# Optimization experiments

Measured on AMD Instinct MI355X. Metric: run time of the kernel, lower is better.

Reference implementation:

```python
import jax, jax.numpy as jnp
import numpy as np

EMBED_DIM = 768
NUM_HEADS = 12
HEAD_DIM = EMBED_DIM // NUM_HEADS
B, N = 4, 2048


def setup_inputs() -> dict:
    key = jax.random.key(0)
    k_x, k_wqkv, k_bqkv, k_wo, k_bo = jax.random.split(key, 5)
    s = 1.0 / np.sqrt(EMBED_DIM)
    return {
        "x": jax.random.normal(k_x, (B, N, EMBED_DIM), dtype=jnp.float32),
        # torch nn.Linear weight layout: [out_features, in_features]
        "w_qkv": jax.random.uniform(k_wqkv, (3 * EMBED_DIM, EMBED_DIM), minval=-s, maxval=s, dtype=jnp.float32),
        "b_qkv": jax.random.uniform(k_bqkv, (3 * EMBED_DIM,), minval=-s, maxval=s, dtype=jnp.float32),
        "w_out": jax.random.uniform(k_wo, (EMBED_DIM, EMBED_DIM), minval=-s, maxval=s, dtype=jnp.float32),
        "b_out": jax.random.uniform(k_bo, (EMBED_DIM,), minval=-s, maxval=s, dtype=jnp.float32),
    }


def reference(x, w_qkv, b_qkv, w_out, b_out):
    Bsz, Nlen, C = x.shape
    # fused QKV projection: [B, N, 3C]
    qkv = jnp.einsum("bnc,oc->bno", x, w_qkv) + b_qkv
    qkv = qkv.reshape(Bsz, Nlen, 3, NUM_HEADS, HEAD_DIM)
    q = qkv[:, :, 0].transpose(0, 2, 1, 3)  # [B, H, N, D]
    k = qkv[:, :, 1].transpose(0, 2, 1, 3)
    v = qkv[:, :, 2].transpose(0, 2, 1, 3)
    scale = 1.0 / np.sqrt(HEAD_DIM).astype(np.float32)
    scores = jnp.einsum("bhqd,bhkd->bhqk", q, k) * scale  # [B, H, N, N]
    attn = jax.nn.softmax(scores, axis=-1)
    ctx = jnp.einsum("bhqk,bhkd->bhqd", attn, v)  # [B, H, N, D]
    ctx = ctx.transpose(0, 2, 1, 3).reshape(Bsz, Nlen, C)
    return jnp.einsum("bnc,oc->bno", ctx, w_out) + b_out
```

## Files before the change

### kernel.cpp

```cpp
#include <hip/hip_runtime.h>
#include <math.h>

typedef __attribute__((ext_vector_type(8))) short bf16x8;
typedef __attribute__((ext_vector_type(4))) float f32x4;
typedef unsigned short u16;

namespace {
constexpr int BATCH = 4, SEQ = 2048, CDIM = 768, NH = 12, HD = 64;
constexpr int MROWS = BATCH * SEQ;
constexpr int KD = CDIM;
constexpr float QSCALE = 0.125f * 1.44269504088896f;
}

__device__ __forceinline__ u16 f2bf(float f) {
  unsigned x = __float_as_uint(f);
  return (u16)((x + 0x7fffu + ((x >> 16) & 1u)) >> 16);
}

__device__ __forceinline__ unsigned pk2bf(float a, float b) {
  unsigned r;
  asm("v_cvt_pk_bf16_f32 %0, %1, %2" : "=v"(r) : "v"(a), "v"(b));
  return r;
}

__device__ __forceinline__ float exp2asm(float x) {
  float r;
  asm("v_exp_f32 %0, %1" : "=v"(r) : "v"(x));
  return r;
}

#define GLD16(gp, lp)                                                        \
  __builtin_amdgcn_global_load_lds(                                          \
      (const __attribute__((address_space(1))) void*)(gp),                   \
      (__attribute__((address_space(3))) void*)(lp), 16, 0, 0)

__global__ void convert_bf16(const float* __restrict__ x, u16* __restrict__ xb, int nx4,
                             const float* __restrict__ w1, u16* __restrict__ w1b, int n14,
                             const float* __restrict__ w2, u16* __restrict__ w2b, int n24) {
  const int stride = gridDim.x * blockDim.x;
  const int t0 = blockIdx.x * blockDim.x + threadIdx.x;
  for (int i = t0; i < nx4; i += stride) {
    float4 v = ((const float4*)x)[i];
    ushort4 o; o.x = f2bf(v.x); o.y = f2bf(v.y); o.z = f2bf(v.z); o.w = f2bf(v.w);
    ((ushort4*)xb)[i] = o;
  }
  for (int i = t0; i < n14; i += stride) {
    float4 v = ((const float4*)w1)[i];
    ushort4 o; o.x = f2bf(v.x); o.y = f2bf(v.y); o.z = f2bf(v.z); o.w = f2bf(v.w);
    ((ushort4*)w1b)[i] = o;
  }
  for (int i = t0; i < n24; i += stride) {
    float4 v = ((const float4*)w2)[i];
    ushort4 o; o.x = f2bf(v.x); o.y = f2bf(v.y); o.z = f2bf(v.z); o.w = f2bf(v.w);
    ((ushort4*)w2b)[i] = o;
  }
}

template <int MODE>
__global__ __launch_bounds__(512, 4) void gemm_bf16(
    const u16* __restrict__ A, const u16* __restrict__ Bw,
    const float* __restrict__ bias, float* __restrict__ outf,
    u16* __restrict__ qws, u16* __restrict__ kws, u16* __restrict__ vws) {
  __shared__ u16 smem[2 * 128 * 64];
  u16* As = smem;
  u16* Bs = smem + 128 * 64;
  const int t = threadIdx.x;
  const int w = t >> 6, l = t & 63, g = l >> 4, li = l & 15;
  const int wm = w >> 1, wn = w & 1;
  const int lin = blockIdx.x;
  const int rowb = ((lin & 7) << 3) | ((lin >> 3) & 7);
  const int colb = lin >> 6;
  const int row0 = rowb * 128, col0 = colb * 128;

  const int srow = w * 16 + (l >> 3);
  const int skc = (l & 7) ^ (l >> 3);
  const u16* gA = A + (size_t)(row0 + srow) * KD + skc * 8;
  const u16* gB = Bw + (size_t)(col0 + srow) * KD + skc * 8;

  f32x4 acc[2][4];
#pragma unroll
  for (int a = 0; a < 2; ++a)
#pragma unroll
    for (int c = 0; c < 4; ++c) acc[a][c] = {0.f, 0.f, 0.f, 0.f};

#define GSTAGE(k0_)                                                           \
  do {                                                                        \
    _Pragma("unroll")                                                         \
    for (int j = 0; j < 2; ++j) {                                             \
      GLD16(gA + (size_t)8 * j * KD + (k0_), &As[(w * 16 + 8 * j) * 64]);     \
      GLD16(gB + (size_t)8 * j * KD + (k0_), &Bs[(w * 16 + 8 * j) * 64]);     \
    }                                                                         \
  } while (0)

  constexpr int NK = KD / 64;
  for (int kk = 0; kk < NK; ++kk) {
    __syncthreads();
    GSTAGE(kk * 64);
    __syncthreads();

    bf16x8 af[2][2], bfr[4][2];
#pragma unroll
    for (int mi = 0; mi < 2; ++mi) {
      const int r = wm * 32 + mi * 16 + li;
#pragma unroll
      for (int ks = 0; ks < 2; ++ks)
        af[mi][ks] = *(const bf16x8*)&As[r * 64 + (((ks * 4 + g) ^ (li & 7)) * 8)];
    }
#pragma unroll
    for (int ni = 0; ni < 4; ++ni) {
      const int r = wn * 64 + ni * 16 + li;
#pragma unroll
      for (int ks = 0; ks < 2; ++ks)
        bfr[ni][ks] = *(const bf16x8*)&Bs[r * 64 + (((ks * 4 + g) ^ (li & 7)) * 8)];
    }
#pragma unroll
    for (int ni = 0; ni < 4; ++ni)
#pragma unroll
      for (int mi = 0; mi < 2; ++mi) {
        acc[mi][ni] = __builtin_amdgcn_mfma_f32_16x16x32_bf16(af[mi][0], bfr[ni][0], acc[mi][ni], 0, 0, 0);
        acc[mi][ni] = __builtin_amdgcn_mfma_f32_16x16x32_bf16(af[mi][1], bfr[ni][1], acc[mi][ni], 0, 0, 0);
      }
  }
#undef GSTAGE

  float bsr[4];
#pragma unroll
  for (int ni = 0; ni < 4; ++ni) bsr[ni] = bias[col0 + wn * 64 + ni * 16 + li];
  const int bidx = row0 >> 11;
  const int nseq0 = row0 & (SEQ - 1);

  __syncthreads();

  if (MODE == 1) {
    float* Cf = (float*)smem;
#pragma unroll
    for (int p = 0; p < 4; ++p) {
      if (wm == p) {
#pragma unroll
        for (int mi = 0; mi < 2; ++mi)
#pragma unroll
          for (int ni = 0; ni < 4; ++ni)
#pragma unroll
            for (int i = 0; i < 4; ++i)
              Cf[(mi * 16 + 4 * g + i) * 132 + wn * 64 + ni * 16 + li] =
                  acc[mi][ni][i] + bsr[ni];
      }
      __syncthreads();
#pragma unroll
      for (int j = 0; j < 2; ++j) {
        const int fid = t + 512 * j;
        const int r = fid >> 5, c4 = (fid & 31) * 4;
        *(float4*)(outf + (size_t)(row0 + p * 32 + r) * CDIM + col0 + c4) =
            *(const float4*)&Cf[r * 132 + c4];
      }
      __syncthreads();
    }
  } else {
#pragma unroll
    for (int hc = 0; hc < 2; ++hc) {
      const int nb = col0 + hc * 64;
      const int s = nb / CDIM;
      const int h = (nb % CDIM) / HD;
      if (wn == hc) {
        if (s < 2) {
          const float qs = (s == 0) ? QSCALE : 1.f;
#pragma unroll
          for (int mi = 0; mi < 2; ++mi)
#pragma unroll
            for (int ni = 0; ni < 4; ++ni)
#pragma unroll
              for (int i = 0; i < 4; ++i)
                smem[(wm * 32 + mi * 16 + 4 * g + i) * 72 + ni * 16 + li] =
                    f2bf((acc[mi][ni][i] + bsr[ni]) * qs);
        } else {
#pragma unroll
          for (int mi = 0; mi < 2; ++mi)
#pragma unroll
            for (int ni = 0; ni < 4; ++ni)
#pragma unroll
              for (int i = 0; i < 4; ++i)
                smem[(ni * 16 + li) * 136 + wm * 32 + mi * 16 + 4 * g + i] =
                    f2bf(acc[mi][ni][i] + bsr[ni]);
        }
      }
      __syncthreads();
      if (s < 2) {
        u16* dst = (s == 0 ? qws : kws) + ((size_t)(bidx * NH + h) * SEQ + nseq0) * HD;
        const int r = t >> 3, c = (t & 7) * 8;
#pragma unroll
        for (int rd = 0; rd < 2; ++rd)
          *(uint4*)(dst + (size_t)(r + 64 * rd) * HD + c) =
              *(const uint4*)&smem[(r + 64 * rd) * 72 + c];
      } else {
        u16* dst = vws + (size_t)(bidx * NH + h) * HD * SEQ + nseq0;
        const int d = t >> 4, c = (t & 15) * 8;
#pragma unroll
        for (int rd = 0; rd < 2; ++rd)
          *(uint4*)(dst + (size_t)(d + 32 * rd) * SEQ + c) =
              *(const uint4*)&smem[(d + 32 * rd) * 136 + c];
      }
      __syncthreads();
    }
  }
}

__global__ __launch_bounds__(256, 3) void attn_mfma(
    const u16* __restrict__ qws, const u16* __restrict__ kws,
    const u16* __restrict__ vws, u16* __restrict__ ctx) {
  __shared__ u16 Ks[2][64 * 64];
  __shared__ u16 Vs[2][64 * 64];
  __shared__ u16 Ps[4 * 32 * 72];
  const int t = threadIdx.x;
  const int w = t >> 6, l = t & 63, g = l >> 4, li = l & 15;
  const int q0 = blockIdx.x * 128;
  const int h = blockIdx.y, b = blockIdx.z;
  const size_t bh = (size_t)b * NH + h;
  const u16* qb = qws + bh * SEQ * HD;
  const u16* kb = kws + bh * SEQ * HD;
  const u16* vb = vws + bh * HD * SEQ;

  bf16x8 qf[2][2];
#pragma unroll
  for (int qt = 0; qt < 2; ++qt)
#pragma unroll
    for (int ks = 0; ks < 2; ++ks)
      qf[qt][ks] = *(const bf16x8*)(qb + (size_t)(q0 + w * 32 + qt * 16 + li) * HD + ks * 32 + g * 8);
  asm volatile("s_waitcnt vmcnt(0)" ::: "memory");
  __builtin_amdgcn_sched_barrier(0);

  f32x4 acc[4][2];
#pragma unroll
  for (int dt = 0; dt < 4; ++dt)
#pragma unroll
    for (int qt = 0; qt < 2; ++qt) acc[dt][qt] = {0.f, 0.f, 0.f, 0.f};
  float lrun[2] = {0.f, 0.f};

  const int srow8 = l >> 3;
  const int skc = (l & 7) ^ srow8;
  const u16* gK = kb + (size_t)(w * 16 + srow8) * HD + skc * 8;
  const u16* gV = vb + (size_t)(w * 16 + srow8) * SEQ + skc * 8;
  u16* Pw = Ps + w * 32 * 72;

  constexpr int NT = SEQ / 64;

#define STAGE(kt_, buf_)                                                          \
  do {                                                                            \
    const int key0_ = (kt_) * 64;                                                 \
    GLD16(gK + (size_t)(key0_ + 0) * HD, &Ks[buf_][(w * 16 + 0) * 64]);           \
    GLD16(gV + (size_t)0 * SEQ + key0_, &Vs[buf_][(w * 16 + 0) * 64]);            \
    GLD16(gK + (size_t)(key0_ + 8) * HD, &Ks[buf_][(w * 16 + 8) * 64]);           \
    GLD16(gV + (size_t)8 * SEQ + key0_, &Vs[buf_][(w * 16 + 8) * 64]);            \
  } while (0)

  STAGE(0, 0);
  STAGE(1, 1);
  asm volatile("s_waitcnt vmcnt(4)" ::: "memory");
  __builtin_amdgcn_sched_barrier(0);
  __builtin_amdgcn_s_barrier();
  __builtin_amdgcn_sched_barrier(0);

  const f32x4 Z = {0.f, 0.f, 0.f, 0.f};

  for (int kt = 0; kt < NT; ++kt) {
    const int cur = kt & 1;
    const u16* KsC = Ks[cur];
    const u16* VsC = Vs[cur];

    f32x4 S[4][2];
    __builtin_amdgcn_s_setprio(1);
#pragma unroll
    for (int kb4 = 0; kb4 < 4; ++kb4) {
      bf16x8 kf0 = *(const bf16x8*)&KsC[(kb4 * 16 + li) * 64 + ((g ^ (li & 7)) * 8)];
      bf16x8 kf1 = *(const bf16x8*)&KsC[(kb4 * 16 + li) * 64 + (((4 + g) ^ (li & 7)) * 8)];
#pragma unroll
      for (int qt = 0; qt < 2; ++qt) {
        S[kb4][qt] = __builtin_amdgcn_mfma_f32_16x16x32_bf16(kf0, qf[qt][0], Z, 0, 0, 0);
        S[kb4][qt] = __builtin_amdgcn_mfma_f32_16x16x32_bf16(kf1, qf[qt][1], S[kb4][qt], 0, 0, 0);
      }
    }
    __builtin_amdgcn_s_setprio(0);

#pragma unroll
    for (int qt = 0; qt < 2; ++qt) {
      float rs = 0.f;
#pragma unroll
      for (int kb4 = 0; kb4 < 4; ++kb4) {
        const float p0 = exp2asm(S[kb4][qt][0]);
        const float p1 = exp2asm(S[kb4][qt][1]);
        const float p2 = exp2asm(S[kb4][qt][2]);
        const float p3 = exp2asm(S[kb4][qt][3]);
        rs += (p0 + p1) + (p2 + p3);
        uint2 pk;
        pk.x = pk2bf(p0, p1);
        pk.y = pk2bf(p2, p3);
        *(uint2*)&Pw[(qt * 16 + li) * 72 + ((kb4 ^ (li & 3)) * 16) + 4 * g] = pk;
      }
      lrun[qt] += rs;
    }

    bf16x8 vf[4][2];
#pragma unroll
    for (int dt = 0; dt < 4; ++dt) {
      vf[dt][0] = *(const bf16x8*)&VsC[(dt * 16 + li) * 64 + ((g ^ (li & 7)) * 8)];
      vf[dt][1] = *(const bf16x8*)&VsC[(dt * 16 + li) * 64 + (((4 + g) ^ (li & 7)) * 8)];
    }
    bf16x8 pf[2][2];
#pragma unroll
    for (int qt = 0; qt < 2; ++qt)
#pragma unroll
      for (int ks = 0; ks < 2; ++ks) {
        const int slot = (ks * 2 + (g >> 1)) ^ (li & 3);
        pf[qt][ks] = *(const bf16x8*)&Pw[(qt * 16 + li) * 72 + slot * 16 + (g & 1) * 8];
      }

    __builtin_amdgcn_s_setprio(1);
#pragma unroll
    for (int dt = 0; dt < 4; ++dt)
#pragma unroll
      for (int qt = 0; qt < 2; ++qt) {
        acc[dt][qt] = __builtin_amdgcn_mfma_f32_16x16x32_bf16(vf[dt][0], pf[qt][0], acc[dt][qt], 0, 0, 0);
        acc[dt][qt] = __builtin_amdgcn_mfma_f32_16x16x32_bf16(vf[dt][1], pf[qt][1], acc[dt][qt], 0, 0, 0);
      }
    __builtin_amdgcn_s_setprio(0);

    if (kt + 1 < NT) {
      asm volatile("s_waitcnt vmcnt(0)" ::: "memory");
      __builtin_amdgcn_sched_barrier(0);
      __builtin_amdgcn_s_barrier();
      __builtin_amdgcn_sched_barrier(0);
      if (kt + 2 < NT) STAGE(kt + 2, cur);
    }
  }
#undef STAGE

#pragma unroll
  for (int qt = 0; qt < 2; ++qt) {
    lrun[qt] += __shfl_xor(lrun[qt], 16);
    lrun[qt] += __shfl_xor(lrun[qt], 32);
  }
  float inv[2] = {1.f / lrun[0], 1.f / lrun[1]};
#pragma unroll
  for (int qt = 0; qt < 2; ++qt)
#pragma unroll
    for (int dt = 0; dt < 4; ++dt) {
      uint2 pk;
      pk.x = pk2bf(acc[dt][qt][0] * inv[qt], acc[dt][qt][1] * inv[qt]);
      pk.y = pk2bf(acc[dt][qt][2] * inv[qt], acc[dt][qt][3] * inv[qt]);
      *(uint2*)&Ps[(w * 32 + qt * 16 + li) * 72 + dt * 16 + 4 * g] = pk;
    }
  __syncthreads();
  {
    const int r = t >> 3, c = (t & 7) * 8;
#pragma unroll
    for (int rd = 0; rd < 4; ++rd)
      *(uint4*)(ctx + ((size_t)b * SEQ + q0 + r + 32 * rd) * CDIM + h * HD + c) =
          *(const uint4*)&Ps[(r + 32 * rd) * 72 + c];
  }
}

extern "C" void kernel_launch(void* const* d_in, const int* in_sizes, int n_in,
                              void* d_out, int out_size, void* d_ws, size_t ws_size,
                              hipStream_t stream) {
  (void)in_sizes; (void)n_in; (void)out_size; (void)ws_size;
  const float* x     = (const float*)d_in[0];
  const float* w_qkv = (const float*)d_in[1];
  const float* b_qkv = (const float*)d_in[2];
  const float* w_out = (const float*)d_in[3];
  const float* b_out = (const float*)d_in[4];
  float* out = (float*)d_out;

  u16* xb    = (u16*)d_ws;
  u16* wqkvb = xb + (size_t)MROWS * KD;
  u16* wob   = wqkvb + (size_t)3 * CDIM * KD;
  u16* qb    = wob + (size_t)CDIM * KD;
  const size_t QS = (size_t)BATCH * NH * SEQ * HD;
  u16* kb   = qb + QS;
  u16* vb   = kb + QS;
  u16* ctxb = vb + QS;

  hipLaunchKernelGGL(convert_bf16, dim3(2048), dim3(256), 0, stream,
                     x, xb, MROWS * KD / 4,
                     w_qkv, wqkvb, 3 * CDIM * KD / 4,
                     w_out, wob, CDIM * KD / 4);
  hipLaunchKernelGGL((gemm_bf16<0>), dim3((MROWS / 128) * (3 * CDIM / 128)), dim3(512), 0,
                     stream, xb, wqkvb, b_qkv, nullptr, qb, kb, vb);
  hipLaunchKernelGGL(attn_mfma, dim3(SEQ / 128, NH, BATCH), dim3(256), 0, stream,
                     qb, kb, vb, ctxb);
  hipLaunchKernelGGL((gemm_bf16<1>), dim3((MROWS / 128) * (CDIM / 128)), dim3(512), 0,
                     stream, ctxb, wob, b_out, out, nullptr, nullptr, nullptr);
}
```

Before: 203.7 us.

## Double-buffer GEMM LDS tiles with async prefetch and use exp2 builtin

The bf16 GEMM now keeps two LDS stages and prefetches tile kt+2 with global_load_lds while MFMAs run on the current tile. This replaces the per-iteration load-then-compute pattern with two barriers, so global latency can overlap with compute. It also raises MFMA priority around the compute block. The attention softmax switches from inline-asm v_exp_f32 to the compiler's exp2 builtin, which lets the scheduler interleave it with other work. Doubling LDS to 64KB per block lowers how many blocks fit on a CU, so the occupancy implied by the launch bounds is no longer reachable.

```diff
diff --git a/kernel.cpp b/kernel.cpp
--- a/kernel.cpp
+++ b/kernel.cpp
@@ -23,11 +23,14 @@
   return r;
 }
 
-__device__ __forceinline__ float exp2asm(float x) {
-  float r;
-  asm("v_exp_f32 %0, %1" : "=v"(r) : "v"(x));
-  return r;
-}
+#if defined(__has_builtin)
+#if __has_builtin(__builtin_amdgcn_exp2f)
+#define EXP2(x) __builtin_amdgcn_exp2f(x)
+#endif
+#endif
+#ifndef EXP2
+#define EXP2(x) exp2f(x)
+#endif
 
 #define GLD16(gp, lp)                                                        \
   __builtin_amdgcn_global_load_lds(                                          \
@@ -61,9 +64,7 @@
     const u16* __restrict__ A, const u16* __restrict__ Bw,
     const float* __restrict__ bias, float* __restrict__ outf,
     u16* __restrict__ qws, u16* __restrict__ kws, u16* __restrict__ vws) {
-  __shared__ u16 smem[2 * 128 * 64];
-  u16* As = smem;
-  u16* Bs = smem + 128 * 64;
+  __shared__ u16 smem[2 * 2 * 128 * 64];
   const int t = threadIdx.x;
   const int w = t >> 6, l = t & 63, g = l >> 4, li = l & 15;
   const int wm = w >> 1, wn = w & 1;
@@ -83,20 +84,30 @@
 #pragma unroll
     for (int c = 0; c < 4; ++c) acc[a][c] = {0.f, 0.f, 0.f, 0.f};
 
-#define GSTAGE(k0_)                                                           \
+#define GSTAGE(kt_, buf_)                                                     \
   do {                                                                        \
+    const int k0_ = (kt_) * 64;                                               \
+    u16* As_ = smem + (buf_) * (2 * 128 * 64);                                \
+    u16* Bs_ = As_ + 128 * 64;                                                \
     _Pragma("unroll")                                                         \
     for (int j = 0; j < 2; ++j) {                                             \
-      GLD16(gA + (size_t)8 * j * KD + (k0_), &As[(w * 16 + 8 * j) * 64]);     \
-      GLD16(gB + (size_t)8 * j * KD + (k0_), &Bs[(w * 16 + 8 * j) * 64]);     \
+      GLD16(gA + (size_t)8 * j * KD + k0_, &As_[(w * 16 + 8 * j) * 64]);      \
+      GLD16(gB + (size_t)8 * j * KD + k0_, &Bs_[(w * 16 + 8 * j) * 64]);      \
     }                                                                         \
   } while (0)
 
   constexpr int NK = KD / 64;
-  for (int kk = 0; kk < NK; ++kk) {
-    __syncthreads();
-    GSTAGE(kk * 64);
-    __syncthreads();
+  GSTAGE(0, 0);
+  GSTAGE(1, 1);
+  asm volatile("s_waitcnt vmcnt(4)" ::: "memory");
+  __builtin_amdgcn_sched_barrier(0);
+  __builtin_amdgcn_s_barrier();
+  __builtin_amdgcn_sched_barrier(0);
+
+  for (int kt = 0; kt < NK; ++kt) {
+    const int cur = kt & 1;
+    const u16* AsC = smem + cur * (2 * 128 * 64);
+    const u16* BsC = AsC + 128 * 64;
 
     bf16x8 af[2][2], bfr[4][2];
 #pragma unroll
@@ -104,15 +115,16 @@
       const int r = wm * 32 + mi * 16 + li;
 #pragma unroll
       for (int ks = 0; ks < 2; ++ks)
-        af[mi][ks] = *(const bf16x8*)&As[r * 64 + (((ks * 4 + g) ^ (li & 7)) * 8)];
+        af[mi][ks] = *(const bf16x8*)&AsC[r * 64 + (((ks * 4 + g) ^ (li & 7)) * 8)];
     }
 #pragma unroll
     for (int ni = 0; ni < 4; ++ni) {
       const int r = wn * 64 + ni * 16 + li;
 #pragma unroll
       for (int ks = 0; ks < 2; ++ks)
-        bfr[ni][ks] = *(const bf16x8*)&Bs[r * 64 + (((ks * 4 + g) ^ (li & 7)) * 8)];
-    }
+        bfr[ni][ks] = *(const bf16x8*)&BsC[r * 64 + (((ks * 4 + g) ^ (li & 7)) * 8)];
+    }
+    __builtin_amdgcn_s_setprio(1);
 #pragma unroll
     for (int ni = 0; ni < 4; ++ni)
 #pragma unroll
@@ -120,6 +132,15 @@
         acc[mi][ni] = __builtin_amdgcn_mfma_f32_16x16x32_bf16(af[mi][0], bfr[ni][0], acc[mi][ni], 0, 0, 0);
         acc[mi][ni] = __builtin_amdgcn_mfma_f32_16x16x32_bf16(af[mi][1], bfr[ni][1], acc[mi][ni], 0, 0, 0);
       }
+    __builtin_amdgcn_s_setprio(0);
+
+    if (kt + 1 < NK) {
+      asm volatile("s_waitcnt vmcnt(0)" ::: "memory");
+      __builtin_amdgcn_sched_barrier(0);
+      __builtin_amdgcn_s_barrier();
+      __builtin_amdgcn_sched_barrier(0);
+      if (kt + 2 < NK) GSTAGE(kt + 2, cur);
+    }
   }
 #undef GSTAGE
 
@@ -285,10 +306,10 @@
       float rs = 0.f;
 #pragma unroll
       for (int kb4 = 0; kb4 < 4; ++kb4) {
-        const float p0 = exp2asm(S[kb4][qt][0]);
-        const float p1 = exp2asm(S[kb4][qt][1]);
-        const float p2 = exp2asm(S[kb4][qt][2]);
-        const float p3 = exp2asm(S[kb4][qt][3]);
+        const float p0 = EXP2(S[kb4][qt][0]);
+        const float p1 = EXP2(S[kb4][qt][1]);
+        const float p2 = EXP2(S[kb4][qt][2]);
+        const float p3 = EXP2(S[kb4][qt][3]);
         rs += (p0 + p1) + (p2 + p3);
         uint2 pk;
         pk.x = pk2bf(p0, p1);
```

New measurement: 196.2 us. -3.7%, faster.
